# Kernel optimization log

Measured on AMD Instinct MI355X. Metric: run time of the kernel, lower is better.

## Reference

```python
import jax, jax.numpy as jnp
import numpy as np

B, T, EPROJS = 32, 512, 512
DUNITS, ODIM, ATT_DIM = 1024, 10000, 320
L = 128
SOS = EOS = ODIM - 1
SCALING = 2.0  # espnet AttDot scaling
LOGZERO = -1e10


def setup_inputs() -> dict:
    key = jax.random.key(0)
    ks = jax.random.split(key, 12)
    s = 0.02
    inp = {}
    inp["hs_pad"] = jax.random.normal(ks[0], (B, T, EPROJS), jnp.float32)
    inp["hlens"] = jax.random.randint(ks[1], (B,), T // 2, T + 1)
    inp["ys_pad"] = jax.random.randint(ks[2], (B, L), 1, ODIM - 1)
    # embedding
    inp["embed_w"] = jax.random.normal(ks[3], (ODIM, DUNITS), jnp.float32) * s
    # AttDot params: mlp_enc (eprojs->att_dim, bias), mlp_dec (dunits->att_dim, no bias)
    inp["Wenc"] = jax.random.normal(ks[4], (ATT_DIM, EPROJS), jnp.float32) * s
    inp["benc"] = jnp.zeros((ATT_DIM,), jnp.float32)
    inp["Wdec"] = jax.random.normal(ks[5], (ATT_DIM, DUNITS), jnp.float32) * s
    # LSTMCell layer 0: input = dunits + eprojs
    inp["W_ih0"] = jax.random.normal(ks[6], (4 * DUNITS, DUNITS + EPROJS), jnp.float32) * s
    inp["W_hh0"] = jax.random.normal(ks[7], (4 * DUNITS, DUNITS), jnp.float32) * s
    inp["b_ih0"] = jnp.zeros((4 * DUNITS,), jnp.float32)
    inp["b_hh0"] = jnp.zeros((4 * DUNITS,), jnp.float32)
    # LSTMCell layer 1: input = dunits
    inp["W_ih1"] = jax.random.normal(ks[8], (4 * DUNITS, DUNITS), jnp.float32) * s
    inp["W_hh1"] = jax.random.normal(ks[9], (4 * DUNITS, DUNITS), jnp.float32) * s
    inp["b_ih1"] = jnp.zeros((4 * DUNITS,), jnp.float32)
    inp["b_hh1"] = jnp.zeros((4 * DUNITS,), jnp.float32)
    # output projection (context_residual=False -> dunits -> odim)
    inp["Wout"] = jax.random.normal(ks[10], (ODIM, DUNITS), jnp.float32) * s
    inp["bout"] = jnp.zeros((ODIM,), jnp.float32)
    return inp


def _lstm_cell(x, h, c, Wih, Whh, bih, bhh):
    g = x @ Wih.T + bih + h @ Whh.T + bhh
    i, f, gg, o = jnp.split(g, 4, axis=-1)  # torch gate order i,f,g,o
    c2 = jax.nn.sigmoid(f) * c + jax.nn.sigmoid(i) * jnp.tanh(gg)
    h2 = jax.nn.sigmoid(o) * jnp.tanh(c2)
    return h2, c2


def reference(hs_pad, hlens, ys_pad, embed_w, Wenc, benc, Wdec,
              W_ih0, W_hh0, b_ih0, b_hh0, W_ih1, W_hh1, b_ih1, b_hh1,
              Wout, bout):
    Bm, Lm = ys_pad.shape
    ys_in = jnp.concatenate([jnp.full((Bm, 1), SOS, ys_pad.dtype), ys_pad], axis=1)   # [B, L+1]
    ys_out = jnp.concatenate([ys_pad, jnp.full((Bm, 1), EOS, ys_pad.dtype)], axis=1)  # [B, L+1]
    eys = embed_w[ys_in]  # [B, L+1, dunits]

    # AttDot: cache tanh(mlp_enc(h)) once; mask by hlens
    pre_enc = jnp.tanh(jnp.einsum('btd,ad->bta', hs_pad, Wenc) + benc)  # [B, T, A]
    mask = jnp.arange(hs_pad.shape[1])[None, :] < hlens[:, None]        # [B, T]

    zc0 = jnp.zeros((Bm, DUNITS), hs_pad.dtype)
    carry0 = (zc0, zc0, zc0, zc0)  # z0, c0, z1, c1

    def step(carry, ey_t):
        z0, c0, z1, c1 = carry
        dec = jnp.tanh(z0 @ Wdec.T)                            # [B, A]
        e = jnp.einsum('bta,ba->bt', pre_enc, dec)             # [B, T]
        w = jax.nn.softmax(jnp.where(mask, SCALING * e, LOGZERO), axis=-1)
        att_c = jnp.einsum('bt,btd->bd', w, hs_pad)            # [B, eprojs]
        ey = jnp.concatenate([ey_t, att_c], axis=-1)           # [B, dunits+eprojs]
        z0, c0 = _lstm_cell(ey, z0, c0, W_ih0, W_hh0, b_ih0, b_hh0)
        z1, c1 = _lstm_cell(z0, z1, c1, W_ih1, W_hh1, b_ih1, b_hh1)
        return (z0, c0, z1, c1), z1

    _, zs = jax.lax.scan(step, carry0, jnp.swapaxes(eys, 0, 1))  # [L+1, B, dunits]
    zs = jnp.swapaxes(zs, 0, 1)                                  # [B, L+1, dunits]

    logits = jnp.einsum('bld,od->blo', zs, Wout) + bout          # [B, L+1, odim]
    logp = jax.nn.log_softmax(logits, axis=-1)
    nll = -jnp.take_along_axis(logp, ys_out[..., None], axis=-1)[..., 0]
    # F.cross_entropy mean over all tokens (no ignore_id padding present),
    # then scaled by (mean len(ys_in) - 1) == L
    loss = nll.mean() * Lm
    acc = jnp.mean((jnp.argmax(logits, axis=-1) == ys_out).astype(jnp.float32))
    # ppl = exp(loss * mean(len_in) / sum(len_in)) = exp(loss / B)
    ppl = jnp.exp(loss / Bm)
    return loss, acc, ppl
```

## Files before the change

### kernel.cpp

```cpp
#include <hip/hip_runtime.h>
#include <hip/hip_fp16.h>
#include <math.h>


typedef _Float16 f16;
typedef _Float16 f16x2 __attribute__((ext_vector_type(2)));
typedef _Float16 f16x4 __attribute__((ext_vector_type(4)));
typedef _Float16 f16x8 __attribute__((ext_vector_type(8)));
typedef float f32x4 __attribute__((ext_vector_type(4)));

#define SOS_ID 9999
#define NB 32
#define NTT 512
#define NE 512
#define ND 1024
#define NA 320
#define NO 10000
#define NL 129
#define NTOK (NL*NB)
#define NG0 256
#define NG1 128
#define GRID_LOOP 416

#define S_SZ0  0
#define R_SZ0  16
#define S_SZ1  17
#define R_SZ1  25
#define S_SATT 26
#define R_SATT 30
#define S_SDEC 31
#define R_SDEC 35
#define F_SZ0  64
#define F_SZ1  80
#define F_SATT 88
#define F_SDEC 104

union PU32 { unsigned u; f16x2 h; };
union PU64 { unsigned long long u; f16x4 h; unsigned w[2]; };

__device__ __forceinline__ float fdot2f(f16x2 a, f16x2 b, float c) {
#if __has_builtin(__builtin_amdgcn_fdot2)
  return __builtin_amdgcn_fdot2(a, b, c, false);
#else
  return c + (float)a[0]*(float)b[0] + (float)a[1]*(float)b[1];
#endif
}
__device__ __forceinline__ float dot8(f16x8 a, f16x8 b, float acc) {
  acc = fdot2f(__builtin_shufflevector(a, a, 0, 1), __builtin_shufflevector(b, b, 0, 1), acc);
  acc = fdot2f(__builtin_shufflevector(a, a, 2, 3), __builtin_shufflevector(b, b, 2, 3), acc);
  acc = fdot2f(__builtin_shufflevector(a, a, 4, 5), __builtin_shufflevector(b, b, 4, 5), acc);
  acc = fdot2f(__builtin_shufflevector(a, a, 6, 7), __builtin_shufflevector(b, b, 6, 7), acc);
  return acc;
}
__device__ __forceinline__ float sigf(float x) { return 1.0f / (1.0f + __expf(-x)); }
__device__ __forceinline__ float tanhf_fast(float x) { return 1.0f - 2.0f / (1.0f + __expf(2.0f * x)); }

__device__ __forceinline__ unsigned long long aload64(const void* p) {
  return __hip_atomic_load((const unsigned long long*)p, __ATOMIC_RELAXED, __HIP_MEMORY_SCOPE_AGENT);
}
__device__ __forceinline__ void astore32(void* p, unsigned v) {
  __hip_atomic_store((unsigned*)p, v, __ATOMIC_RELAXED, __HIP_MEMORY_SCOPE_AGENT);
}
__device__ __forceinline__ unsigned pack2(float a, float b) {
  PU32 u; u.h[0] = (f16)a; u.h[1] = (f16)b; return u.u;
}

__device__ __forceinline__ void sigstep(unsigned* bar, int sub, unsigned subtgt,
                                        int root, unsigned roottgt,
                                        int flag0, int nrep, unsigned val) {
  unsigned old = __hip_atomic_fetch_add(&bar[sub * 32], 1u, __ATOMIC_RELEASE, __HIP_MEMORY_SCOPE_AGENT);
  if (old + 1u == subtgt) {
    unsigned r = __hip_atomic_fetch_add(&bar[root * 32], 1u, __ATOMIC_RELEASE, __HIP_MEMORY_SCOPE_AGENT);
    if (r + 1u == roottgt) {
      for (int i = 0; i < nrep; ++i)
        __hip_atomic_store(&bar[(flag0 + i) * 32], val, __ATOMIC_RELEASE, __HIP_MEMORY_SCOPE_AGENT);
    }
  }
}
__device__ __forceinline__ void waitflag(unsigned* bar, int slot, unsigned val) {
  if (threadIdx.x == 0) {
    while (__hip_atomic_load(&bar[slot * 32], __ATOMIC_RELAXED, __HIP_MEMORY_SCOPE_AGENT) < val)
      __builtin_amdgcn_s_sleep(1);
  }
  __syncthreads();
  asm volatile("" ::: "memory");
}

__global__ void k_cvt(const float* __restrict__ s, f16* __restrict__ d, long n) {
  long i = (long)blockIdx.x * 256 + threadIdx.x;
  long st = (long)gridDim.x * 256;
  for (; i < n; i += st) d[i] = (f16)s[i];
}
__global__ void k_w0cat(const float* __restrict__ wih, const float* __restrict__ whh, f16* __restrict__ dst) {
  int j = blockIdx.y; int k = blockIdx.x * 256 + threadIdx.x;
  float v;
  if (k < 1024)      v = wih[(long)j * 1536 + k];
  else if (k < 2048) v = whh[(long)j * 1024 + (k - 1024)];
  else               v = wih[(long)j * 1536 + 1024 + (k - 2048)];
  dst[(long)j * 2560 + k] = (f16)v;
}
__global__ void k_w1cat(const float* __restrict__ wih, const float* __restrict__ whh, f16* __restrict__ dst) {
  int j = blockIdx.y; int k = blockIdx.x * 256 + threadIdx.x;
  float v = (k < 1024) ? wih[(long)j * 1024 + k] : whh[(long)j * 1024 + (k - 1024)];
  dst[(long)j * 2048 + k] = (f16)v;
}
__global__ void k_eys(const int* __restrict__ ys, const float* __restrict__ emb, f16* __restrict__ eys) {
  int sb = blockIdx.y; int k = blockIdx.x * 256 + threadIdx.x;
  int s = sb >> 5, b = sb & 31;
  int tok = (s == 0) ? SOS_ID : ys[b * 128 + (s - 1)];
  eys[(long)sb * 1024 + k] = (f16)emb[(long)tok * 1024 + k];
}
__global__ void k_pre(const f16* __restrict__ hs, const f16* __restrict__ wenc,
                      const float* __restrict__ benc, f16* __restrict__ preT) {
  const int row0 = blockIdx.x * 32;
  for (int idx = threadIdx.x; idx < 32 * NA; idx += 256) {
    int r = row0 + idx / NA, a = idx % NA;
    const f16x8* hp = (const f16x8*)(hs + (long)r * NE);
    const f16x8* wp = (const f16x8*)(wenc + (long)a * NE);
    float acc = 0.f;
#pragma unroll 4
    for (int k = 0; k < 64; ++k) acc = dot8(hp[k], wp[k], acc);
    int b = r >> 9, t = r & 511;
    preT[((long)b * NA + a) * 512 + t] = (f16)tanhf_fast(acc + benc[a]);
  }
}
__global__ void k_bias(const float* a0, const float* b0, const float* a1, const float* b1,
                       float* s0, float* s1) {
  int i = blockIdx.x * 256 + threadIdx.x;
  if (i < 4096) { s0[i] = a0[i] + b0[i]; s1[i] = a1[i] + b1[i]; }
}
__global__ void k_zero(f16* dec, float* scal, unsigned* bar) {
  int i = blockIdx.x * 256 + threadIdx.x;
  if (i < NB * NA) dec[i] = (f16)0.f;
  if (i < 4096) bar[i] = 0u;
  if (i < 8) scal[i] = 0.f;
}

struct LoopP {
  const f16 *preT, *hs, *eys, *w0, *w1, *wdec;
  const float *bs0, *bs1;
  const int* hlens;
  f16 *dec, *att, *z0seq, *zout;
  unsigned* bar;
};

__global__ void __launch_bounds__(256, 2) k_loop(LoopP p) {
  __shared__ __align__(16) f16 xs[2][32 * 520];
  __shared__ float gacc[2176];
  __shared__ float cbuf[256];

  const int bid = blockIdx.x, tid = threadIdx.x;
  const int wid = tid >> 6, lane = tid & 63, lr = lane & 15, lq = lane >> 4;
  cbuf[tid] = 0.f;
  __syncthreads();

  auto stage = [&](f16* dst, const f16* src, long rs, bool atomic) {
    for (int idx = tid; idx < 4096; idx += 256) {
      int r = idx >> 7, c = idx & 127;
      const void* sp = (const void*)(src + (long)r * rs + c * 4);
      unsigned long long v = atomic ? aload64(sp) : *(const unsigned long long*)sp;
      *(unsigned long long*)(dst + r * 520 + c * 4) = v;
    }
  };

  if (bid < NG0) {
    const int par = wid;
    const f16* wb = p.w0 + (long)((lr >> 2) * 1024 + bid * 4 + (lr & 3)) * 2560 + lq * 8;
    f16x8 wr[20];
#pragma unroll
    for (int r = 0; r < 20; ++r) {
      const int c = (r < 16) ? ((r >> 2) * 16 + (r & 3) * 4 + par)
                             : (64 + (r - 16) * 4 + par);
      wr[r] = *(const f16x8*)(wb + c * 32);
    }
#pragma unroll
    for (int r = 0; r < 20; ++r) asm volatile("" : "+v"(wr[r]));
    const bool decduty = (bid < 20);
    const int a0 = bid * 16;
    const f16* wdrow = p.wdec + (long)(a0 + lr) * ND + lq * 8;
    const f16* a00 = xs[0] + lr * 520 + lq * 8;
    const f16* a01 = a00 + 16 * 520;
    const f16* a10 = xs[1] + lr * 520 + lq * 8;
    const f16* a11 = a10 + 16 * 520;
    const float* bs = p.bs0;

    stage(xs[0], p.eys, ND, false);
    stage(xs[1], p.eys + 512, ND, false);
    __syncthreads();

    for (int s = 0; s < NL; ++s) {
      f32x4 acc0 = (f32x4){0.f, 0.f, 0.f, 0.f};
      f32x4 acc1 = (f32x4){0.f, 0.f, 0.f, 0.f};
#pragma unroll
      for (int j = 0; j < 4; ++j) {
        const int co = (4 * j + par) * 32;
        acc0 = __builtin_amdgcn_mfma_f32_16x16x32_f16(*(const f16x8*)(a00 + co), wr[j], acc0, 0, 0, 0);
        acc1 = __builtin_amdgcn_mfma_f32_16x16x32_f16(*(const f16x8*)(a01 + co), wr[j], acc1, 0, 0, 0);
      }
#pragma unroll
      for (int j = 0; j < 4; ++j) {
        const int co = (4 * j + par) * 32;
        acc0 = __builtin_amdgcn_mfma_f32_16x16x32_f16(*(const f16x8*)(a10 + co), wr[4 + j], acc0, 0, 0, 0);
        acc1 = __builtin_amdgcn_mfma_f32_16x16x32_f16(*(const f16x8*)(a11 + co), wr[4 + j], acc1, 0, 0, 0);
      }
      __syncthreads();
      if (s > 0) {
        waitflag(p.bar, F_SZ0 + (bid & 15), (unsigned)s);
        stage(xs[0], p.z0seq + (long)(s - 1) * (NB * ND), ND, true);
        stage(xs[1], p.z0seq + (long)(s - 1) * (NB * ND) + 512, ND, true);
        __syncthreads();
#pragma unroll
        for (int j = 0; j < 4; ++j) {
          const int co = (4 * j + par) * 32;
          acc0 = __builtin_amdgcn_mfma_f32_16x16x32_f16(*(const f16x8*)(a00 + co), wr[8 + j], acc0, 0, 0, 0);
          acc1 = __builtin_amdgcn_mfma_f32_16x16x32_f16(*(const f16x8*)(a01 + co), wr[8 + j], acc1, 0, 0, 0);
        }
#pragma unroll
        for (int j = 0; j < 4; ++j) {
          const int co = (4 * j + par) * 32;
          acc0 = __builtin_amdgcn_mfma_f32_16x16x32_f16(*(const f16x8*)(a10 + co), wr[12 + j], acc0, 0, 0, 0);
          acc1 = __builtin_amdgcn_mfma_f32_16x16x32_f16(*(const f16x8*)(a11 + co), wr[12 + j], acc1, 0, 0, 0);
        }
        __syncthreads();
      }
      waitflag(p.bar, F_SATT + (bid & 15), (unsigned)(s + 1));
      stage(xs[0], p.att, NE, true);
      __syncthreads();
#pragma unroll
      for (int j = 0; j < 4; ++j) {
        const int co = (4 * j + par) * 32;
        acc0 = __builtin_amdgcn_mfma_f32_16x16x32_f16(*(const f16x8*)(a00 + co), wr[16 + j], acc0, 0, 0, 0);
        acc1 = __builtin_amdgcn_mfma_f32_16x16x32_f16(*(const f16x8*)(a01 + co), wr[16 + j], acc1, 0, 0, 0);
      }
#pragma unroll
      for (int reg = 0; reg < 4; ++reg) {
        gacc[par * 544 + (lq * 4 + reg) * 17 + lr]      = acc0[reg];
        gacc[par * 544 + (16 + lq * 4 + reg) * 17 + lr] = acc1[reg];
      }
      __syncthreads();
      if (tid < 64) {
        const int b = tid & 31, q = tid >> 5;
        float z[2];
#pragma unroll
        for (int u = 0; u < 2; ++u) {
          const int hh = q * 2 + u;
          float gi = 0.f, gf = 0.f, gv = 0.f, go = 0.f;
#pragma unroll
          for (int pp = 0; pp < 4; ++pp) {
            const float* gp = gacc + pp * 544 + b * 17;
            gi += gp[hh]; gf += gp[4 + hh]; gv += gp[8 + hh]; go += gp[12 + hh];
          }
          const int hb = bid * 4 + hh;
          gi += bs[hb]; gf += bs[1024 + hb]; gv += bs[2048 + hb]; go += bs[3072 + hb];
          float cn = sigf(gf) * cbuf[b * 4 + hh] + sigf(gi) * tanhf_fast(gv);
          cbuf[b * 4 + hh] = cn;
          z[u] = sigf(go) * tanhf_fast(cn);
        }
        astore32((unsigned*)p.z0seq + ((long)s * (NB * ND) + b * ND + bid * 4) / 2 + q,
                 pack2(z[0], z[1]));
      }
      __syncthreads();
      if (tid == 0)
        sigstep(p.bar, S_SZ0 + (bid & 15), 16u * (s + 1), R_SZ0, 16u * (s + 1),
                F_SZ0, 16, (unsigned)(s + 1));
      if (decduty) {
        waitflag(p.bar, F_SZ0 + (bid & 15), (unsigned)(s + 1));
        stage(xs[0], p.z0seq + (long)s * (NB * ND), ND, true);
        stage(xs[1], p.z0seq + (long)s * (NB * ND) + 512, ND, true);
        __syncthreads();
        f32x4 dacc = (f32x4){0.f, 0.f, 0.f, 0.f};
        if (wid < 2) {
#pragma unroll
          for (int kt = 0; kt < 2; ++kt) {
            const f16* ap2 = xs[kt] + (wid * 16 + lr) * 520 + lq * 8;
            const f16* wk = wdrow + kt * 512;
#pragma unroll
            for (int kk = 0; kk < 512; kk += 32)
              dacc = __builtin_amdgcn_mfma_f32_16x16x32_f16(
                  *(const f16x8*)(ap2 + kk), *(const f16x8*)(wk + kk), dacc, 0, 0, 0);
          }
        }
        __syncthreads();
        if (wid < 2) {
#pragma unroll
          for (int reg = 0; reg < 4; ++reg)
            gacc[(wid * 16 + lq * 4 + reg) * 33 + lr] = tanhf_fast(dacc[reg]);
        }
        __syncthreads();
        {
          const int b = tid & 31, j = tid >> 5;
          astore32((unsigned*)p.dec + (b * NA + a0) / 2 + j,
                   pack2(gacc[b * 33 + 2 * j], gacc[b * 33 + 2 * j + 1]));
        }
        __syncthreads();
        if (tid == 0)
          sigstep(p.bar, S_SDEC + (bid & 3), 5u * (s + 1), R_SDEC, 4u * (s + 1),
                  F_SDEC, 8, (unsigned)(s + 1));
      }
      if (s + 1 < NL) {
        stage(xs[0], p.eys + (long)(s + 1) * (NB * ND), ND, false);
        stage(xs[1], p.eys + (long)(s + 1) * (NB * ND) + 512, ND, false);
      }
      __syncthreads();
    }
  } else if (bid < NG0 + NG1) {
    const int g1i = bid - NG0;
    const int rt = wid & 1, par = wid >> 1;
    const int rrow = rt * 16 + lr;
    const f16* wb = p.w1 + (long)((rrow >> 3) * 1024 + g1i * 8 + (rrow & 7)) * 2048 + lq * 8;
    f16x8 wr[32];
#pragma unroll
    for (int r = 0; r < 32; ++r) {
      const int c = (r < 16) ? ((r >> 3) * 16 + (r & 7) * 2 + par)
                             : (32 + ((r - 16) >> 3) * 16 + ((r - 16) & 7) * 2 + par);
      wr[r] = *(const f16x8*)(wb + c * 32);
    }
#pragma unroll
    for (int r = 0; r < 32; ++r) asm volatile("" : "+v"(wr[r]));
    const f16* a00 = xs[0] + lr * 520 + lq * 8;
    const f16* a01 = a00 + 16 * 520;
    const f16* a10 = xs[1] + lr * 520 + lq * 8;
    const f16* a11 = a10 + 16 * 520;
    const float* bs = p.bs1;
    const int h0 = g1i * 8;

    for (int s = 0; s < NL; ++s) {
      f32x4 acc0 = (f32x4){0.f, 0.f, 0.f, 0.f};
      f32x4 acc1 = (f32x4){0.f, 0.f, 0.f, 0.f};
      if (s > 0) {
        waitflag(p.bar, F_SZ1 + (g1i & 7), (unsigned)s);
        stage(xs[0], p.zout + (long)(s - 1) * (NB * ND), ND, true);
        stage(xs[1], p.zout + (long)(s - 1) * (NB * ND) + 512, ND, true);
        __syncthreads();
#pragma unroll
        for (int j = 0; j < 8; ++j) {
          const int co = (2 * j + par) * 32;
          acc0 = __builtin_amdgcn_mfma_f32_16x16x32_f16(*(const f16x8*)(a00 + co), wr[16 + j], acc0, 0, 0, 0);
          acc1 = __builtin_amdgcn_mfma_f32_16x16x32_f16(*(const f16x8*)(a01 + co), wr[16 + j], acc1, 0, 0, 0);
        }
#pragma unroll
        for (int j = 0; j < 8; ++j) {
          const int co = (2 * j + par) * 32;
          acc0 = __builtin_amdgcn_mfma_f32_16x16x32_f16(*(const f16x8*)(a10 + co), wr[24 + j], acc0, 0, 0, 0);
          acc1 = __builtin_amdgcn_mfma_f32_16x16x32_f16(*(const f16x8*)(a11 + co), wr[24 + j], acc1, 0, 0, 0);
        }
        __syncthreads();
      }
      waitflag(p.bar, F_SZ0 + (bid & 15), (unsigned)(s + 1));
      stage(xs[0], p.z0seq + (long)s * (NB * ND), ND, true);
      stage(xs[1], p.z0seq + (long)s * (NB * ND) + 512, ND, true);
      __syncthreads();
#pragma unroll
      for (int j = 0; j < 8; ++j) {
        const int co = (2 * j + par) * 32;
        acc0 = __builtin_amdgcn_mfma_f32_16x16x32_f16(*(const f16x8*)(a00 + co), wr[j], acc0, 0, 0, 0);
        acc1 = __builtin_amdgcn_mfma_f32_16x16x32_f16(*(const f16x8*)(a01 + co), wr[j], acc1, 0, 0, 0);
      }
#pragma unroll
      for (int j = 0; j < 8; ++j) {
        const int co = (2 * j + par) * 32;
        acc0 = __builtin_amdgcn_mfma_f32_16x16x32_f16(*(const f16x8*)(a10 + co), wr[8 + j], acc0, 0, 0, 0);
        acc1 = __builtin_amdgcn_mfma_f32_16x16x32_f16(*(const f16x8*)(a11 + co), wr[8 + j], acc1, 0, 0, 0);
      }
#pragma unroll
      for (int reg = 0; reg < 4; ++reg) {
        gacc[par * 1056 + (lq * 4 + reg) * 33 + rrow]      = acc0[reg];
        gacc[par * 1056 + (16 + lq * 4 + reg) * 33 + rrow] = acc1[reg];
      }
      __syncthreads();
      if (tid < 128) {
        const int b = tid & 31, hp = tid >> 5;
        float z[2];
#pragma unroll
        for (int u = 0; u < 2; ++u) {
          const int hh = hp * 2 + u;
          float gi = gacc[b * 33 + hh]      + gacc[1056 + b * 33 + hh]      + bs[h0 + hh];
          float gf = gacc[b * 33 + 8 + hh]  + gacc[1056 + b * 33 + 8 + hh]  + bs[1024 + h0 + hh];
          float gv = gacc[b * 33 + 16 + hh] + gacc[1056 + b * 33 + 16 + hh] + bs[2048 + h0 + hh];
          float go = gacc[b * 33 + 24 + hh] + gacc[1056 + b * 33 + 24 + hh] + bs[3072 + h0 + hh];
          float cn = sigf(gf) * cbuf[b * 8 + hh] + sigf(gi) * tanhf_fast(gv);
          cbuf[b * 8 + hh] = cn;
          z[u] = sigf(go) * tanhf_fast(cn);
        }
        astore32((unsigned*)p.zout + ((long)s * (NB * ND) + b * ND + h0) / 2 + hp,
                 pack2(z[0], z[1]));
      }
      __syncthreads();
      if (tid == 0)
        sigstep(p.bar, S_SZ1 + (g1i & 7), 16u * (s + 1), R_SZ1, 8u * (s + 1),
                F_SZ1, 8, (unsigned)(s + 1));
    }
  } else {
    const int b = bid - (NG0 + NG1);
    const int hlen = p.hlens[b];
    float* epart = (float*)xs;
    float* apart = (float*)xs + 2048;
    float* wL    = (float*)xs + 4096;
    float* decF  = gacc;
    float* red   = cbuf;
    const f16* pe  = p.preT + (long)b * NA * 512;
    const f16* ph  = p.hs   + (long)b * 512 * 512;

    for (int s = 0; s < NL; ++s) {
      if (s > 0) waitflag(p.bar, F_SDEC + (b & 7), (unsigned)s);
      if (tid < 80) {
        PU64 v; v.u = aload64((const unsigned long long*)p.dec + b * 80 + tid);
#pragma unroll
        for (int i = 0; i < 4; ++i) decF[tid * 4 + i] = (float)v.h[i];
      }
      __syncthreads();
      {
        float ea[8] = {0.f,0.f,0.f,0.f,0.f,0.f,0.f,0.f};
#pragma unroll 8
        for (int aa = 0; aa < 80; ++aa) {
          const int a = wid * 80 + aa;
          f16x8 pv = *(const f16x8*)(pe + (long)a * 512 + lane * 8);
          const float d = decF[a];
#pragma unroll
          for (int j = 0; j < 8; ++j) ea[j] += (float)pv[j] * d;
        }
#pragma unroll
        for (int j = 0; j < 8; ++j) epart[wid * 512 + lane * 8 + j] = ea[j];
      }
      __syncthreads();
      const int t0 = 2 * tid, t1 = 2 * tid + 1;
      float e0 = (epart[t0] + epart[512 + t0] + epart[1024 + t0] + epart[1536 + t0]) * 2.0f;
      float e1 = (epart[t1] + epart[512 + t1] + epart[1024 + t1] + epart[1536 + t1]) * 2.0f;
      float m = fmaxf((t0 < hlen) ? e0 : -3e38f, (t1 < hlen) ? e1 : -3e38f);
#pragma unroll
      for (int off = 1; off < 64; off <<= 1) m = fmaxf(m, __shfl_xor(m, off));
      if (lane == 0) red[wid] = m;
      __syncthreads();
      const float M = fmaxf(fmaxf(red[0], red[1]), fmaxf(red[2], red[3]));
      float w0 = (t0 < hlen) ? __expf(e0 - M) : 0.f;
      float w1 = (t1 < hlen) ? __expf(e1 - M) : 0.f;
      wL[t0] = w0; wL[t1] = w1;
      float sm = w0 + w1;
#pragma unroll
      for (int off = 1; off < 64; off <<= 1) sm += __shfl_xor(sm, off);
      __syncthreads();
      if (lane == 0) red[wid] = sm;
      __syncthreads();
      const float inv = 1.0f / (red[0] + red[1] + red[2] + red[3]);
      {
        float ac[8] = {0.f,0.f,0.f,0.f,0.f,0.f,0.f,0.f};
#pragma unroll 8
        for (int tt = 0; tt < 128; ++tt) {
          const int t = wid * 128 + tt;
          f16x8 hv = *(const f16x8*)(ph + (long)t * 512 + lane * 8);
          const float w = wL[t];
#pragma unroll
          for (int j = 0; j < 8; ++j) ac[j] += (float)hv[j] * w;
        }
#pragma unroll
        for (int j = 0; j < 8; ++j) apart[wid * 512 + lane * 8 + j] = ac[j];
      }
      __syncthreads();
      {
        float s0 = apart[t0] + apart[512 + t0] + apart[1024 + t0] + apart[1536 + t0];
        float s1 = apart[t1] + apart[512 + t1] + apart[1024 + t1] + apart[1536 + t1];
        astore32((unsigned*)p.att + b * 256 + tid, pack2(s0 * inv, s1 * inv));
      }
      __syncthreads();
      if (tid == 0)
        sigstep(p.bar, S_SATT + (b & 3), 8u * (s + 1), R_SATT, 4u * (s + 1),
                F_SATT, 16, (unsigned)(s + 1));
    }
  }
}

__global__ void __launch_bounds__(256) k_lgemm(const f16* __restrict__ z, const f16* __restrict__ wout,
                                               const float* __restrict__ bout, float4* __restrict__ part) {
  const int mb = blockIdx.x, nb = blockIdx.y;
  const int wid = threadIdx.x >> 6, lane = threadIdx.x & 63;
  const int lr = lane & 15, lq = lane >> 4;
  const int m0 = mb * 32;
  const int n0 = nb * 512 + wid * 128;
  const f16* arow0 = z + (long)(m0 + lr) * 1024 + lq * 8;
  const f16* arow1 = arow0 + (long)16 * 1024;
  const f16* bp[8];
  int cols[8];
#pragma unroll
  for (int nt = 0; nt < 8; ++nt) {
    int n = n0 + nt * 16 + lr;
    cols[nt] = n;
    int nc = (n < NO) ? n : (NO - 1);
    bp[nt] = wout + (long)nc * 1024 + lq * 8;
  }
  f32x4 acc[16];
#pragma unroll
  for (int i = 0; i < 16; ++i) acc[i] = (f32x4){0.f, 0.f, 0.f, 0.f};
  for (int kk = 0; kk < 1024; kk += 32) {
    f16x8 a0v = *(const f16x8*)(arow0 + kk);
    f16x8 a1v = *(const f16x8*)(arow1 + kk);
#pragma unroll
    for (int nt = 0; nt < 8; ++nt) {
      f16x8 bv = *(const f16x8*)(bp[nt] + kk);
      acc[nt]     = __builtin_amdgcn_mfma_f32_16x16x32_f16(a0v, bv, acc[nt], 0, 0, 0);
      acc[8 + nt] = __builtin_amdgcn_mfma_f32_16x16x32_f16(a1v, bv, acc[8 + nt], 0, 0, 0);
    }
  }
  float bias[8];
#pragma unroll
  for (int nt = 0; nt < 8; ++nt) bias[nt] = (cols[nt] < NO) ? bout[cols[nt]] : 0.f;
  const int chunk = nb * 4 + wid;
#pragma unroll
  for (int mt = 0; mt < 2; ++mt) {
#pragma unroll
    for (int reg = 0; reg < 4; ++reg) {
      float vals[8];
      float mx = -1e30f, av = -1e30f; int ai = 0;
#pragma unroll
      for (int nt = 0; nt < 8; ++nt) {
        float v = (cols[nt] < NO) ? (acc[mt * 8 + nt][reg] + bias[nt]) : -1e30f;
        vals[nt] = v;
        mx = fmaxf(mx, v);
        if (v > av) { av = v; ai = cols[nt]; }
      }
      float sum = 0.f;
#pragma unroll
      for (int nt = 0; nt < 8; ++nt) sum += (vals[nt] > -9e29f) ? __expf(vals[nt] - mx) : 0.f;
#pragma unroll
      for (int off = 1; off < 16; off <<= 1) {
        float mo = __shfl_xor(mx, off);
        float so = __shfl_xor(sum, off);
        float avo = __shfl_xor(av, off);
        int aio = __shfl_xor(ai, off);
        float nm = fmaxf(mx, mo);
        float e1 = (mx > -9e29f) ? __expf(mx - nm) : 0.f;
        float e2 = (mo > -9e29f) ? __expf(mo - nm) : 0.f;
        sum = sum * e1 + so * e2;
        mx = nm;
        if (avo > av || (avo == av && aio < ai)) { av = avo; ai = aio; }
      }
      if (lr == 0) {
        int rowg = m0 + mt * 16 + lq * 4 + reg;
        float4 q; q.x = mx; q.y = sum; q.z = av; q.w = __int_as_float(ai);
        part[(long)rowg * 80 + chunk] = q;
      }
    }
  }
}

__global__ void k_tl(const f16* __restrict__ z, const f16* __restrict__ wout,
                     const float* __restrict__ bout, const int* __restrict__ ys, float* __restrict__ tl) {
  const int tok = blockIdx.x * 4 + (threadIdx.x >> 6);
  const int lane = threadIdx.x & 63;
  if (tok >= NTOK) return;
  const int s = tok >> 5, b = tok & 31;
  const int tgt = (s < 128) ? ys[b * 128 + s] : SOS_ID;
  const f16x8* zp = (const f16x8*)(z + (long)tok * 1024);
  const f16x8* wp = (const f16x8*)(wout + (long)tgt * 1024);
  float acc = 0.f;
  acc = dot8(zp[lane], wp[lane], acc);
  acc = dot8(zp[64 + lane], wp[64 + lane], acc);
#pragma unroll
  for (int off = 32; off > 0; off >>= 1) acc += __shfl_xor(acc, off);
  if (lane == 0) tl[tok] = acc + bout[tgt];
}

__global__ void k_ce(const float4* __restrict__ part, const float* __restrict__ tl,
                     const int* __restrict__ ys, float* scal) {
  const int m = blockIdx.x * 256 + threadIdx.x;
  float nll = 0.f, okf = 0.f;
  if (m < NTOK) {
    float M = -1e30f, S = 0.f, av = -1e30f; int ai = 0;
    for (int c = 0; c < 80; ++c) {
      float4 q = part[(long)m * 80 + c];
      float qm = q.x, qs = q.y, qa = q.z; int qi = __float_as_int(q.w);
      float nm = fmaxf(M, qm);
      float e1 = (M > -9e29f) ? __expf(M - nm) : 0.f;
      float e2 = (qm > -9e29f) ? __expf(qm - nm) : 0.f;
      S = S * e1 + qs * e2; M = nm;
      if (qa > av || (qa == av && qi < ai)) { av = qa; ai = qi; }
    }
    float lse = M + __logf(S);
    int s = m >> 5, b = m & 31;
    int tgt = (s < 128) ? ys[b * 128 + s] : SOS_ID;
    nll = lse - tl[m];
    okf = (ai == tgt) ? 1.f : 0.f;
  }
  __shared__ float r1[256], r2[256];
  r1[threadIdx.x] = nll; r2[threadIdx.x] = okf; __syncthreads();
  for (int st = 128; st > 0; st >>= 1) {
    if (threadIdx.x < st) { r1[threadIdx.x] += r1[threadIdx.x + st]; r2[threadIdx.x] += r2[threadIdx.x + st]; }
    __syncthreads();
  }
  if (threadIdx.x == 0) { atomicAdd(&scal[0], r1[0]); atomicAdd(&scal[1], r2[0]); }
}

__global__ void k_final(const float* scal, float* out) {
  if (threadIdx.x == 0) {
    float loss = scal[0] * (128.f / 4128.f);
    out[0] = loss;
    out[1] = scal[1] * (1.f / 4128.f);
    out[2] = expf(loss / 32.f);
  }
}

extern "C" void kernel_launch(void* const* d_in, const int* in_sizes, int n_in,
                              void* d_out, int out_size, void* d_ws, size_t ws_size,
                              hipStream_t stream) {
  const float* hs_pad = (const float*)d_in[0];
  const int* hlens    = (const int*)d_in[1];
  const int* ys_pad   = (const int*)d_in[2];
  const float* embed  = (const float*)d_in[3];
  const float* Wenc   = (const float*)d_in[4];
  const float* benc   = (const float*)d_in[5];
  const float* Wdec   = (const float*)d_in[6];
  const float* Wih0   = (const float*)d_in[7];
  const float* Whh0   = (const float*)d_in[8];
  const float* bih0   = (const float*)d_in[9];
  const float* bhh0   = (const float*)d_in[10];
  const float* Wih1   = (const float*)d_in[11];
  const float* Whh1   = (const float*)d_in[12];
  const float* bih1   = (const float*)d_in[13];
  const float* bhh1   = (const float*)d_in[14];
  const float* Wout   = (const float*)d_in[15];
  const float* bout   = (const float*)d_in[16];
  float* out = (float*)d_out;
  (void)in_sizes; (void)n_in; (void)out_size; (void)ws_size;

  char* ws = (char*)d_ws;
  size_t off = 0;
  auto alloc = [&](size_t bytes) -> char* {
    char* pp = ws + off;
    off = (off + bytes + 255) & ~(size_t)255;
    return pp;
  };
  f16* hs16    = (f16*)alloc((size_t)NB * NTT * NE * 2);
  f16* preT    = (f16*)alloc((size_t)NB * NA * NTT * 2);
  f16* eys16   = (f16*)alloc((size_t)NL * NB * ND * 2);
  f16* w0cat   = (f16*)alloc((size_t)4096 * 2560 * 2);
  f16* w1cat   = (f16*)alloc((size_t)4096 * 2048 * 2);
  f16* wdec16  = (f16*)alloc((size_t)NA * ND * 2);
  f16* wenc16  = (f16*)alloc((size_t)NA * NE * 2);
  f16* wout16  = (f16*)alloc((size_t)NO * ND * 2);
  f16* zout    = (f16*)alloc((size_t)NTOK * ND * 2);
  f16* z0seq   = (f16*)alloc((size_t)NL * NB * ND * 2);
  f16* dec16   = (f16*)alloc((size_t)NB * NA * 2);
  f16* att16   = (f16*)alloc((size_t)NB * NE * 2);
  float* bs0   = (float*)alloc(4096 * 4);
  float* bs1   = (float*)alloc(4096 * 4);
  float* tl    = (float*)alloc((size_t)NTOK * 4);
  float4* part = (float4*)alloc((size_t)NTOK * 80 * 16);
  float* scal  = (float*)alloc(256);
  unsigned* bar = (unsigned*)alloc(16384);

  k_cvt<<<dim3(2048), dim3(256), 0, stream>>>(hs_pad, hs16, (long)NB * NTT * NE);
  k_cvt<<<dim3(256), dim3(256), 0, stream>>>(Wdec, wdec16, (long)NA * ND);
  k_cvt<<<dim3(128), dim3(256), 0, stream>>>(Wenc, wenc16, (long)NA * NE);
  k_cvt<<<dim3(2048), dim3(256), 0, stream>>>(Wout, wout16, (long)NO * ND);
  k_w0cat<<<dim3(10, 4096), dim3(256), 0, stream>>>(Wih0, Whh0, w0cat);
  k_w1cat<<<dim3(8, 4096), dim3(256), 0, stream>>>(Wih1, Whh1, w1cat);
  k_eys<<<dim3(4, NL * NB), dim3(256), 0, stream>>>(ys_pad, embed, eys16);
  k_pre<<<dim3(512), dim3(256), 0, stream>>>(hs16, wenc16, benc, preT);
  k_bias<<<dim3(16), dim3(256), 0, stream>>>(bih0, bhh0, bih1, bhh1, bs0, bs1);
  k_zero<<<dim3(128), dim3(256), 0, stream>>>(dec16, scal, bar);

  LoopP lp;
  lp.preT = preT; lp.hs = hs16; lp.eys = eys16; lp.w0 = w0cat; lp.w1 = w1cat; lp.wdec = wdec16;
  lp.bs0 = bs0; lp.bs1 = bs1; lp.hlens = hlens;
  lp.dec = dec16; lp.att = att16; lp.z0seq = z0seq; lp.zout = zout; lp.bar = bar;
  k_loop<<<dim3(GRID_LOOP), dim3(256), 0, stream>>>(lp);

  k_tl<<<dim3(NTOK / 4), dim3(256), 0, stream>>>(zout, wout16, bout, ys_pad, tl);
  k_lgemm<<<dim3(129, 20), dim3(256), 0, stream>>>(zout, wout16, bout, part);
  k_ce<<<dim3(17), dim3(256), 0, stream>>>(part, tl, ys_pad, scal);
  k_final<<<dim3(1), dim3(64), 0, stream>>>(scal, out);
}
```

Measured before the change: 6.707 ms.

## Fuse decoder projection into attention blocks, drop dec barrier stage, trim masked context loop

Removes the separate decoder-projection stage, which had 20 LSTM-0 blocks wait for z0, compute Wdec·z0 and signal a barrier. Each attention block now reads z0 of the previous step itself and computes its own 320-wide tanh(Wdec·z) with dot products. This drops one inter-block synchronisation hop per step at the cost of redundant Wdec reads per batch block. It also skips masked time steps in the context sum and relaxes the barrier atomics to relaxed ordering after an explicit vmcnt wait, which carries some memory-ordering risk.

```diff
diff --git a/kernel.cpp b/kernel.cpp
--- a/kernel.cpp
+++ b/kernel.cpp
@@ -28,12 +28,9 @@
 #define R_SZ1  25
 #define S_SATT 26
 #define R_SATT 30
-#define S_SDEC 31
-#define R_SDEC 35
 #define F_SZ0  64
 #define F_SZ1  80
 #define F_SATT 88
-#define F_SDEC 104
 
 union PU32 { unsigned u; f16x2 h; };
 union PU64 { unsigned long long u; f16x4 h; unsigned w[2]; };
@@ -68,12 +65,13 @@
 __device__ __forceinline__ void sigstep(unsigned* bar, int sub, unsigned subtgt,
                                         int root, unsigned roottgt,
                                         int flag0, int nrep, unsigned val) {
-  unsigned old = __hip_atomic_fetch_add(&bar[sub * 32], 1u, __ATOMIC_RELEASE, __HIP_MEMORY_SCOPE_AGENT);
+  asm volatile("s_waitcnt vmcnt(0)" ::: "memory");
+  unsigned old = __hip_atomic_fetch_add(&bar[sub * 32], 1u, __ATOMIC_RELAXED, __HIP_MEMORY_SCOPE_AGENT);
   if (old + 1u == subtgt) {
-    unsigned r = __hip_atomic_fetch_add(&bar[root * 32], 1u, __ATOMIC_RELEASE, __HIP_MEMORY_SCOPE_AGENT);
+    unsigned r = __hip_atomic_fetch_add(&bar[root * 32], 1u, __ATOMIC_RELAXED, __HIP_MEMORY_SCOPE_AGENT);
     if (r + 1u == roottgt) {
       for (int i = 0; i < nrep; ++i)
-        __hip_atomic_store(&bar[(flag0 + i) * 32], val, __ATOMIC_RELEASE, __HIP_MEMORY_SCOPE_AGENT);
+        __hip_atomic_store(&bar[(flag0 + i) * 32], val, __ATOMIC_RELAXED, __HIP_MEMORY_SCOPE_AGENT);
     }
   }
 }
@@ -129,9 +127,8 @@
   int i = blockIdx.x * 256 + threadIdx.x;
   if (i < 4096) { s0[i] = a0[i] + b0[i]; s1[i] = a1[i] + b1[i]; }
 }
-__global__ void k_zero(f16* dec, float* scal, unsigned* bar) {
+__global__ void k_zero(float* scal, unsigned* bar) {
   int i = blockIdx.x * 256 + threadIdx.x;
-  if (i < NB * NA) dec[i] = (f16)0.f;
   if (i < 4096) bar[i] = 0u;
   if (i < 8) scal[i] = 0.f;
 }
@@ -140,7 +137,7 @@
   const f16 *preT, *hs, *eys, *w0, *w1, *wdec;
   const float *bs0, *bs1;
   const int* hlens;
-  f16 *dec, *att, *z0seq, *zout;
+  f16 *att, *z0seq, *zout;
   unsigned* bar;
 };
 
@@ -175,9 +172,6 @@
     }
 #pragma unroll
     for (int r = 0; r < 20; ++r) asm volatile("" : "+v"(wr[r]));
-    const bool decduty = (bid < 20);
-    const int a0 = bid * 16;
-    const f16* wdrow = p.wdec + (long)(a0 + lr) * ND + lq * 8;
     const f16* a00 = xs[0] + lr * 520 + lq * 8;
     const f16* a01 = a00 + 16 * 520;
     const f16* a10 = xs[1] + lr * 520 + lq * 8;
@@ -263,40 +257,6 @@
       if (tid == 0)
         sigstep(p.bar, S_SZ0 + (bid & 15), 16u * (s + 1), R_SZ0, 16u * (s + 1),
                 F_SZ0, 16, (unsigned)(s + 1));
-      if (decduty) {
-        waitflag(p.bar, F_SZ0 + (bid & 15), (unsigned)(s + 1));
-        stage(xs[0], p.z0seq + (long)s * (NB * ND), ND, true);
-        stage(xs[1], p.z0seq + (long)s * (NB * ND) + 512, ND, true);
-        __syncthreads();
-        f32x4 dacc = (f32x4){0.f, 0.f, 0.f, 0.f};
-        if (wid < 2) {
-#pragma unroll
-          for (int kt = 0; kt < 2; ++kt) {
-            const f16* ap2 = xs[kt] + (wid * 16 + lr) * 520 + lq * 8;
-            const f16* wk = wdrow + kt * 512;
-#pragma unroll
-            for (int kk = 0; kk < 512; kk += 32)
-              dacc = __builtin_amdgcn_mfma_f32_16x16x32_f16(
-                  *(const f16x8*)(ap2 + kk), *(const f16x8*)(wk + kk), dacc, 0, 0, 0);
-          }
-        }
-        __syncthreads();
-        if (wid < 2) {
-#pragma unroll
-          for (int reg = 0; reg < 4; ++reg)
-            gacc[(wid * 16 + lq * 4 + reg) * 33 + lr] = tanhf_fast(dacc[reg]);
-        }
-        __syncthreads();
-        {
-          const int b = tid & 31, j = tid >> 5;
-          astore32((unsigned*)p.dec + (b * NA + a0) / 2 + j,
-                   pack2(gacc[b * 33 + 2 * j], gacc[b * 33 + 2 * j + 1]));
-        }
-        __syncthreads();
-        if (tid == 0)
-          sigstep(p.bar, S_SDEC + (bid & 3), 5u * (s + 1), R_SDEC, 4u * (s + 1),
-                  F_SDEC, 8, (unsigned)(s + 1));
-      }
       if (s + 1 < NL) {
         stage(xs[0], p.eys + (long)(s + 1) * (NB * ND), ND, false);
         stage(xs[1], p.eys + (long)(s + 1) * (NB * ND) + 512, ND, false);
@@ -396,18 +356,42 @@
     float* epart = (float*)xs;
     float* apart = (float*)xs + 2048;
     float* wL    = (float*)xs + 4096;
+    f16*   zbuf  = (f16*)((float*)xs + 4608);
+    float* dred  = (float*)xs + 5120;
     float* decF  = gacc;
     float* red   = cbuf;
     const f16* pe  = p.preT + (long)b * NA * 512;
     const f16* ph  = p.hs   + (long)b * 512 * 512;
 
     for (int s = 0; s < NL; ++s) {
-      if (s > 0) waitflag(p.bar, F_SDEC + (b & 7), (unsigned)s);
-      if (tid < 80) {
-        PU64 v; v.u = aload64((const unsigned long long*)p.dec + b * 80 + tid);
-#pragma unroll
-        for (int i = 0; i < 4; ++i) decF[tid * 4 + i] = (float)v.h[i];
-      }
+      if (s > 0) {
+        waitflag(p.bar, F_SZ0 + (bid & 15), (unsigned)s);
+        unsigned long long v = aload64(
+            (const unsigned long long*)(p.z0seq + (long)(s - 1) * (NB * ND) + (long)b * ND) + tid);
+        *(unsigned long long*)(zbuf + tid * 4) = v;
+      } else {
+        *(unsigned long long*)(zbuf + tid * 4) = 0ull;
+      }
+      __syncthreads();
+      {
+        const f16x8* zb = (const f16x8*)zbuf;
+        const f16x8* wrow = (const f16x8*)(p.wdec + (long)tid * ND);
+        float acc = 0.f;
+#pragma unroll 8
+        for (int k = 0; k < 128; ++k) acc = dot8(wrow[k], zb[k], acc);
+        decF[tid] = tanhf_fast(acc);
+        const int kq = tid & 3;
+        const f16x8* wrow2 = (const f16x8*)(p.wdec + (long)(256 + (tid >> 2)) * ND) + kq * 32;
+        const f16x8* zb2 = zb + kq * 32;
+        float acc2 = 0.f;
+#pragma unroll 8
+        for (int k = 0; k < 32; ++k) acc2 = dot8(wrow2[k], zb2[k], acc2);
+        dred[tid] = acc2;
+      }
+      __syncthreads();
+      if (tid < 64)
+        decF[256 + tid] = tanhf_fast(dred[tid * 4] + dred[tid * 4 + 1] +
+                                     dred[tid * 4 + 2] + dred[tid * 4 + 3]);
       __syncthreads();
       {
         float ea[8] = {0.f,0.f,0.f,0.f,0.f,0.f,0.f,0.f};
@@ -444,9 +428,11 @@
       const float inv = 1.0f / (red[0] + red[1] + red[2] + red[3]);
       {
         float ac[8] = {0.f,0.f,0.f,0.f,0.f,0.f,0.f,0.f};
+        const int tbase = wid * 128;
+        const int tcnt = (hlen > tbase) ? ((hlen - tbase < 128) ? (hlen - tbase) : 128) : 0;
 #pragma unroll 8
-        for (int tt = 0; tt < 128; ++tt) {
-          const int t = wid * 128 + tt;
+        for (int tt = 0; tt < tcnt; ++tt) {
+          const int t = tbase + tt;
           f16x8 hv = *(const f16x8*)(ph + (long)t * 512 + lane * 8);
           const float w = wL[t];
 #pragma unroll
@@ -638,7 +624,6 @@
   f16* wout16  = (f16*)alloc((size_t)NO * ND * 2);
   f16* zout    = (f16*)alloc((size_t)NTOK * ND * 2);
   f16* z0seq   = (f16*)alloc((size_t)NL * NB * ND * 2);
-  f16* dec16   = (f16*)alloc((size_t)NB * NA * 2);
   f16* att16   = (f16*)alloc((size_t)NB * NE * 2);
   float* bs0   = (float*)alloc(4096 * 4);
   float* bs1   = (float*)alloc(4096 * 4);
@@ -656,12 +641,12 @@
   k_eys<<<dim3(4, NL * NB), dim3(256), 0, stream>>>(ys_pad, embed, eys16);
   k_pre<<<dim3(512), dim3(256), 0, stream>>>(hs16, wenc16, benc, preT);
   k_bias<<<dim3(16), dim3(256), 0, stream>>>(bih0, bhh0, bih1, bhh1, bs0, bs1);
-  k_zero<<<dim3(128), dim3(256), 0, stream>>>(dec16, scal, bar);
+  k_zero<<<dim3(128), dim3(256), 0, stream>>>(scal, bar);
 
   LoopP lp;
   lp.preT = preT; lp.hs = hs16; lp.eys = eys16; lp.w0 = w0cat; lp.w1 = w1cat; lp.wdec = wdec16;
   lp.bs0 = bs0; lp.bs1 = bs1; lp.hlens = hlens;
-  lp.dec = dec16; lp.att = att16; lp.z0seq = z0seq; lp.zout = zout; lp.bar = bar;
+  lp.att = att16; lp.z0seq = z0seq; lp.zout = zout; lp.bar = bar;
   k_loop<<<dim3(GRID_LOOP), dim3(256), 0, stream>>>(lp);
 
   k_tl<<<dim3(NTOK / 4), dim3(256), 0, stream>>>(zout, wout16, bout, ys_pad, tl);
```

New measurement: 6.673 ms. Within noise of the previous version (-0.5%).
